# Performance work log

Hardware: AMD Instinct MI355X
Metric: run time of the kernel (lower is better)

## Reference

```python
import jax, jax.numpy as jnp
import numpy as np
from jax import lax

N, L, D = 16, 512, 256
FILT, K = 256, 3
MAXDUR = 8
MEL_MAX = L * (MAXDUR - 1)  # 3584, worst-case sum of durations
LN_EPS = 1e-5


def _conv1d(x, w, b):
    # x: [N, L, Cin], w: [K, Cin, Cout] -> [N, L, Cout], SAME padding (pad=(K-1)//2)
    return lax.conv_general_dilated(x, w, (1,), 'SAME',
                                    dimension_numbers=('NWC', 'WIO', 'NWC')) + b


def _layer_norm(x, g, b):
    mu = jnp.mean(x, axis=-1, keepdims=True)
    var = jnp.var(x, axis=-1, keepdims=True)
    return (x - mu) * lax.rsqrt(var + LN_EPS) * g + b


def _variance_predictor(x, conv1_w, conv1_b, ln1_g, ln1_b,
                        conv2_w, conv2_b, ln2_g, ln2_b, lin_w, lin_b):
    # Standard FastSpeech duration predictor (dropout omitted: eval mode)
    h = _layer_norm(jax.nn.relu(_conv1d(x, conv1_w, conv1_b)), ln1_g, ln1_b)
    h = _layer_norm(jax.nn.relu(_conv1d(h, conv2_w, conv2_b)), ln2_g, ln2_b)
    return (h @ lin_w + lin_b)[..., 0]  # [N, L] log-durations


def setup_inputs() -> dict:
    key = jax.random.key(0)
    ks = jax.random.split(key, 6)
    s = 0.02
    return {
        'x': jax.random.normal(ks[0], (N, L, D), jnp.float32),
        'conv1_w': jax.random.normal(ks[1], (K, D, FILT), jnp.float32) * s,
        'conv1_b': jnp.zeros((FILT,), jnp.float32),
        'ln1_g': jnp.ones((FILT,), jnp.float32),
        'ln1_b': jnp.zeros((FILT,), jnp.float32),
        'conv2_w': jax.random.normal(ks[2], (K, FILT, FILT), jnp.float32) * s,
        'conv2_b': jnp.zeros((FILT,), jnp.float32),
        'ln2_g': jnp.ones((FILT,), jnp.float32),
        'ln2_b': jnp.zeros((FILT,), jnp.float32),
        'lin_w': jax.random.normal(ks[3], (FILT, 1), jnp.float32) * s,
        'lin_b': jnp.zeros((1,), jnp.float32),
        'target': jax.random.randint(ks[4], (N, L), 0, MAXDUR, jnp.int32),
        'mel_max_length': MEL_MAX,
    }


def reference(x, conv1_w, conv1_b, ln1_g, ln1_b, conv2_w, conv2_b,
              ln2_g, ln2_b, lin_w, lin_b, target, mel_max_length):
    log_dur = _variance_predictor(x, conv1_w, conv1_b, ln1_g, ln1_b,
                                  conv2_w, conv2_b, ln2_g, ln2_b, lin_w, lin_b)
    # Dense alignment (faithful to create_alignment), padded directly to mel_max_length
    M = mel_max_length  # static python int
    end = jnp.cumsum(target, axis=1)            # [N, L]
    start = end - target                        # [N, L]
    idx = jnp.arange(M, dtype=target.dtype)[None, :, None]  # [1, M, 1]
    align = ((idx >= start[:, None, :]) & (idx < end[:, None, :])).astype(x.dtype)  # [N, M, L]
    output = jnp.einsum('nml,nld->nmd', align, x)  # [N, M, D]
    return output, log_dur
```

## Files before the change

### kernel.cpp

```cpp
#include <hip/hip_runtime.h>
#include <cstddef>

#define N_ 16
#define L_ 512
#define D_ 256
#define M_ 3584
#define LN_EPS 1e-5f

typedef __attribute__((ext_vector_type(8))) short bf16x8;
typedef __attribute__((ext_vector_type(4))) float f32x4;

__device__ inline unsigned int f2bf_raw(float f) {
    union { float f; unsigned int u; } v; v.f = f;
    return (v.u + 0x7FFFu + ((v.u >> 16) & 1u)) >> 16;
}
__device__ inline unsigned int pack2bf(float lo, float hi) {
    return f2bf_raw(lo) | (f2bf_raw(hi) << 16);
}
__device__ inline float bf2f(unsigned int hw) {
    union { unsigned int u; float f; } v; v.u = hw << 16; return v.f;
}
__device__ inline int aswz(int row, int colb) {
    return row * 512 + (((colb & 0x1F0) ^ ((row & 7) << 4)) | (colb & 0xF));
}

__global__ __launch_bounds__(512)
void prep_kernel(const float* __restrict__ W1, unsigned short* __restrict__ Wt1,
                 const float* __restrict__ W2, unsigned short* __restrict__ Wt2,
                 const int* __restrict__ target, int* __restrict__ idx) {
    __shared__ union { float t[2][32][33]; int s[L_]; } sm;
    const int bid = blockIdx.x;
    if (bid < 192) {
        const int half = threadIdx.x >> 8, st = threadIdx.x & 255;
        const int tile = bid * 2 + half;
        const int kb = (tile % 24) * 32;
        const int cb = ((tile / 24) % 8) * 32;
        const float* W = (tile >= 192) ? W2 : W1;
        unsigned short* Wt = (tile >= 192) ? Wt2 : Wt1;
        const int tx = st & 31, ty = st >> 5;
#pragma unroll
        for (int r = 0; r < 32; r += 8)
            sm.t[half][ty + r][tx] = W[(size_t)(kb + ty + r) * 256 + cb + tx];
        __syncthreads();
        const int jl = st >> 7, l = (st >> 1) & 63, e0 = (st & 1) * 4;
        ushort4 o;
        o.x = (unsigned short)f2bf_raw(sm.t[half][(l >> 4) * 8 + e0 + 0][jl * 16 + (l & 15)]);
        o.y = (unsigned short)f2bf_raw(sm.t[half][(l >> 4) * 8 + e0 + 1][jl * 16 + (l & 15)]);
        o.z = (unsigned short)f2bf_raw(sm.t[half][(l >> 4) * 8 + e0 + 2][jl * 16 + (l & 15)]);
        o.w = (unsigned short)f2bf_raw(sm.t[half][(l >> 4) * 8 + e0 + 3][jl * 16 + (l & 15)]);
        *(ushort4*)(Wt + ((((size_t)(kb >> 5) * 16) + (cb >> 4) + jl) * 64 + l) * 8 + e0) = o;
    } else {
        const int n = bid - 192, t = threadIdx.x;
        const int tv = target[n * L_ + t];
        sm.s[t] = tv;
        __syncthreads();
        for (int off = 1; off < L_; off <<= 1) {
            int v = (t >= off) ? sm.s[t - off] : 0;
            __syncthreads();
            sm.s[t] += v;
            __syncthreads();
        }
        const int e = sm.s[t], st0 = e - tv;
        const int total = sm.s[L_ - 1];
        int* row = idx + (size_t)n * M_;
        for (int j = st0; j < e; ++j) row[j] = t;
        for (int m = total + t; m < M_; m += 512) row[m] = -1;
    }
}

template <int NR, int MAXS>
__device__ __forceinline__ void conv_phase(const unsigned char* Ab,
        const unsigned short* __restrict__ Wf,
        int wv, int lane, int fr, int fg, f32x4 (&acc)[NR][2]) {
    const unsigned short* wb = Wf + ((size_t)(2 * wv) * 64 + lane) * 8;
    uint4 p00 = *(const uint4*)(wb);
    uint4 p01 = *(const uint4*)(wb + 512);
    uint4 p10 = *(const uint4*)(wb + 8192);
    uint4 p11 = *(const uint4*)(wb + 8192 + 512);
    for (int ks = 0; ks < 24; ++ks) {
        uint4 q0, q1;
        if (ks < 22) {
            const unsigned short* wp = wb + (size_t)(ks + 2) * 8192;
            q0 = *(const uint4*)(wp);
            q1 = *(const uint4*)(wp + 512);
        }
        const int cib = (ks & 7) * 64 + fg * 16;
        const int koff = ks >> 3;
        bf16x8 av[NR];
#pragma unroll
        for (int r = 0; r < NR; ++r) {
            int ar = r * 16 + fr + koff;
            if (ar > MAXS) ar = MAXS;
            av[r] = *(const bf16x8*)(Ab + ar * 512 + (cib ^ ((ar & 7) << 4)));
        }
        bf16x8 bb0 = *(bf16x8*)&p00, bb1 = *(bf16x8*)&p01;
        __builtin_amdgcn_s_setprio(1);
#pragma unroll
        for (int r = 0; r < NR; ++r) {
            acc[r][0] = __builtin_amdgcn_mfma_f32_16x16x32_bf16(bb0, av[r], acc[r][0], 0, 0, 0);
            acc[r][1] = __builtin_amdgcn_mfma_f32_16x16x32_bf16(bb1, av[r], acc[r][1], 0, 0, 0);
        }
        __builtin_amdgcn_s_setprio(0);
        p00 = p10; p01 = p11;
        p10 = q0;  p11 = q1;
    }
}

template <int NR, int NROWS>
__device__ __forceinline__ void store_h(unsigned char* Ab, f32x4 (&acc)[NR][2],
        const float* __restrict__ bias, int wv, int fr, int fg) {
#pragma unroll
    for (int r = 0; r < NR; ++r) {
        const int slot = r * 16 + fr;
        if (slot < NROWS) {
#pragma unroll
            for (int j = 0; j < 2; ++j) {
                const int co = wv * 32 + j * 16 + fg * 4;
                const float4 bb = *(const float4*)&bias[co];
                uint2 o;
                o.x = pack2bf(fmaxf(acc[r][j][0] + bb.x, 0.f),
                              fmaxf(acc[r][j][1] + bb.y, 0.f));
                o.y = pack2bf(fmaxf(acc[r][j][2] + bb.z, 0.f),
                              fmaxf(acc[r][j][3] + bb.w, 0.f));
                *(uint2*)(Ab + aswz(slot, 2 * co)) = o;
            }
        }
    }
}

__global__ __launch_bounds__(512, 6)
void mega_kernel(const float* __restrict__ x,
                 const unsigned short* __restrict__ Wf1,
                 const unsigned short* __restrict__ Wf2,
                 const float* __restrict__ b1, const float* __restrict__ g1,
                 const float* __restrict__ be1,
                 const float* __restrict__ b2, const float* __restrict__ g2,
                 const float* __restrict__ be2,
                 const float* __restrict__ lw, const float* __restrict__ lb,
                 const int* __restrict__ idx,
                 float* __restrict__ out0, float* __restrict__ log_dur) {
    __shared__ unsigned char smA[36 * 512];
    const int tid = threadIdx.x, lane = tid & 63, wv = tid >> 6;

    if (blockIdx.x >= 256) {
        const int gb = blockIdx.x - 256;
        const int n = gb >> 5;
        const int m0 = (gb & 31) * 112 + wv;
        const int* ip = idx + (size_t)n * M_ + m0;
        const float* xn = x + (size_t)n * L_ * D_ + lane * 4;
        float* op = out0 + ((size_t)n * M_ + m0) * D_ + lane * 4;
#pragma unroll
        for (int i = 0; i < 7; ++i) {
            const int la = ip[(2 * i) * 8];
            const int lb2 = ip[(2 * i + 1) * 8];
            f32x4 oa = {0.f, 0.f, 0.f, 0.f};
            f32x4 ob = {0.f, 0.f, 0.f, 0.f};
            if (la >= 0)  oa = *(const f32x4*)(xn + (size_t)la * D_);
            if (lb2 >= 0) ob = *(const f32x4*)(xn + (size_t)lb2 * D_);
            __builtin_nontemporal_store(oa, (f32x4*)(op + (size_t)(2 * i) * 8 * D_));
            __builtin_nontemporal_store(ob, (f32x4*)(op + (size_t)(2 * i + 1) * 8 * D_));
        }
        return;
    }

    const int row0 = blockIdx.x * 32;
    const int n = row0 >> 9, l0 = row0 & 511;
    const int fr = lane & 15, fg = lane >> 4;

    for (int i = tid; i < 36 * 64; i += 512) {
        int r = i >> 6, c4 = i & 63;
        int l = l0 - 2 + r;
        float4 v = {0.f, 0.f, 0.f, 0.f};
        if (l >= 0 && l < L_)
            v = ((const float4*)(x + ((size_t)(n * L_ + l)) * D_))[c4];
        uint2 p;
        p.x = pack2bf(v.x, v.y);
        p.y = pack2bf(v.z, v.w);
        *(uint2*)(smA + aswz(r, c4 * 8)) = p;
    }
    __syncthreads();

    f32x4 a1[3][2];
#pragma unroll
    for (int r = 0; r < 3; ++r) { a1[r][0] = (f32x4){0,0,0,0}; a1[r][1] = (f32x4){0,0,0,0}; }
    conv_phase<3, 35>(smA, Wf1, wv, lane, fr, fg, a1);
    __syncthreads();
    store_h<3, 34>(smA, a1, b1, wv, fr, fg);
    __syncthreads();

    {
        const float4 gv = *(const float4*)&g1[lane * 4];
        const float4 bv = *(const float4*)&be1[lane * 4];
        for (int mm = wv; mm < 34; mm += 8) {
            const int addr = aswz(mm, lane * 8);
            const int hrow = l0 - 1 + mm;
            if (hrow < 0 || hrow >= L_) {
                *(uint2*)(smA + addr) = (uint2){0u, 0u};
                continue;
            }
            uint2 pv = *(uint2*)(smA + addr);
            float v0 = bf2f(pv.x & 0xFFFFu), v1 = bf2f(pv.x >> 16);
            float v2 = bf2f(pv.y & 0xFFFFu), v3 = bf2f(pv.y >> 16);
            float s = v0 + v1 + v2 + v3;
            float ss = v0 * v0 + v1 * v1 + v2 * v2 + v3 * v3;
#pragma unroll
            for (int off = 32; off; off >>= 1) {
                s += __shfl_xor(s, off);
                ss += __shfl_xor(ss, off);
            }
            const float mu = s * (1.f / D_);
            const float var = ss * (1.f / D_) - mu * mu;
            const float rs = rsqrtf(var + LN_EPS);
            uint2 o;
            o.x = pack2bf((v0 - mu) * rs * gv.x + bv.x, (v1 - mu) * rs * gv.y + bv.y);
            o.y = pack2bf((v2 - mu) * rs * gv.z + bv.z, (v3 - mu) * rs * gv.w + bv.w);
            *(uint2*)(smA + addr) = o;
        }
    }
    __syncthreads();

    f32x4 a2[2][2];
#pragma unroll
    for (int r = 0; r < 2; ++r) { a2[r][0] = (f32x4){0,0,0,0}; a2[r][1] = (f32x4){0,0,0,0}; }
    conv_phase<2, 33>(smA, Wf2, wv, lane, fr, fg, a2);
    __syncthreads();
    store_h<2, 32>(smA, a2, b2, wv, fr, fg);
    __syncthreads();

    {
        const float4 gv = *(const float4*)&g2[lane * 4];
        const float4 bv = *(const float4*)&be2[lane * 4];
        const float4 wvv = *(const float4*)&lw[lane * 4];
        for (int mm = wv; mm < 32; mm += 8) {
            uint2 pv = *(uint2*)(smA + aswz(mm, lane * 8));
            float v0 = bf2f(pv.x & 0xFFFFu), v1 = bf2f(pv.x >> 16);
            float v2 = bf2f(pv.y & 0xFFFFu), v3 = bf2f(pv.y >> 16);
            float s = v0 + v1 + v2 + v3;
            float ss = v0 * v0 + v1 * v1 + v2 * v2 + v3 * v3;
#pragma unroll
            for (int off = 32; off; off >>= 1) {
                s += __shfl_xor(s, off);
                ss += __shfl_xor(ss, off);
            }
            const float mu = s * (1.f / D_);
            const float var = ss * (1.f / D_) - mu * mu;
            const float rs = rsqrtf(var + LN_EPS);
            float dot = ((v0 - mu) * rs * gv.x + bv.x) * wvv.x
                      + ((v1 - mu) * rs * gv.y + bv.y) * wvv.y
                      + ((v2 - mu) * rs * gv.z + bv.z) * wvv.z
                      + ((v3 - mu) * rs * gv.w + bv.w) * wvv.w;
#pragma unroll
            for (int off = 32; off; off >>= 1) dot += __shfl_xor(dot, off);
            if (lane == 0) log_dur[row0 + mm] = dot + lb[0];
        }
    }
}

extern "C" void kernel_launch(void* const* d_in, const int* in_sizes, int n_in,
                              void* d_out, int out_size, void* d_ws, size_t ws_size,
                              hipStream_t stream) {
    const float* x   = (const float*)d_in[0];
    const float* w1  = (const float*)d_in[1];
    const float* b1  = (const float*)d_in[2];
    const float* g1  = (const float*)d_in[3];
    const float* be1 = (const float*)d_in[4];
    const float* w2  = (const float*)d_in[5];
    const float* b2  = (const float*)d_in[6];
    const float* g2  = (const float*)d_in[7];
    const float* be2 = (const float*)d_in[8];
    const float* lw  = (const float*)d_in[9];
    const float* lb  = (const float*)d_in[10];
    const int* target = (const int*)d_in[11];

    float* out0 = (float*)d_out;
    float* log_dur = out0 + (size_t)N_ * M_ * D_;

    unsigned short* w1f = (unsigned short*)d_ws;
    unsigned short* w2f = w1f + 24 * 8192;
    int* idx = (int*)(w2f + 24 * 8192);

    prep_kernel<<<208, 512, 0, stream>>>(w1, w1f, w2, w2f, target, idx);
    mega_kernel<<<768, 512, 0, stream>>>(x, w1f, w2f, b1, g1, be1,
                                         b2, g2, be2, lw, lb, idx,
                                         out0, log_dur);
}
```

Baseline: 37.21 us.

## Warp-specialize mega kernel: overlap gather writes with conv phases in same block

Result: faster. 33.39 us (-10.3%).

```diff
diff --git a/kernel.cpp b/kernel.cpp
--- a/kernel.cpp
+++ b/kernel.cpp
@@ -128,7 +128,7 @@
     }
 }
 
-__global__ __launch_bounds__(512, 6)
+__global__ __launch_bounds__(1024, 4)
 void mega_kernel(const float* __restrict__ x,
                  const unsigned short* __restrict__ Wf1,
                  const unsigned short* __restrict__ Wf2,
@@ -141,54 +141,57 @@
                  float* __restrict__ out0, float* __restrict__ log_dur) {
     __shared__ unsigned char smA[36 * 512];
     const int tid = threadIdx.x, lane = tid & 63, wv = tid >> 6;
-
-    if (blockIdx.x >= 256) {
-        const int gb = blockIdx.x - 256;
-        const int n = gb >> 5;
-        const int m0 = (gb & 31) * 112 + wv;
-        const int* ip = idx + (size_t)n * M_ + m0;
-        const float* xn = x + (size_t)n * L_ * D_ + lane * 4;
-        float* op = out0 + ((size_t)n * M_ + m0) * D_ + lane * 4;
-#pragma unroll
-        for (int i = 0; i < 7; ++i) {
-            const int la = ip[(2 * i) * 8];
-            const int lb2 = ip[(2 * i + 1) * 8];
-            f32x4 oa = {0.f, 0.f, 0.f, 0.f};
-            f32x4 ob = {0.f, 0.f, 0.f, 0.f};
-            if (la >= 0)  oa = *(const f32x4*)(xn + (size_t)la * D_);
-            if (lb2 >= 0) ob = *(const f32x4*)(xn + (size_t)lb2 * D_);
-            __builtin_nontemporal_store(oa, (f32x4*)(op + (size_t)(2 * i) * 8 * D_));
-            __builtin_nontemporal_store(ob, (f32x4*)(op + (size_t)(2 * i + 1) * 8 * D_));
-        }
-        return;
-    }
-
-    const int row0 = blockIdx.x * 32;
+    const int bid = blockIdx.x;
+    const bool is_conv = (wv < 8);
+
+    const int row0 = bid * 32;
     const int n = row0 >> 9, l0 = row0 & 511;
     const int fr = lane & 15, fg = lane >> 4;
 
-    for (int i = tid; i < 36 * 64; i += 512) {
-        int r = i >> 6, c4 = i & 63;
-        int l = l0 - 2 + r;
-        float4 v = {0.f, 0.f, 0.f, 0.f};
-        if (l >= 0 && l < L_)
-            v = ((const float4*)(x + ((size_t)(n * L_ + l)) * D_))[c4];
-        uint2 p;
-        p.x = pack2bf(v.x, v.y);
-        p.y = pack2bf(v.z, v.w);
-        *(uint2*)(smA + aswz(r, c4 * 8)) = p;
-    }
-    __syncthreads();
+    const int gwv = wv - 8;
+    const int m0 = (bid & 15) * 224 + gwv;
+    const int* ip = idx + (size_t)n * M_ + m0;
+    const float* xn = x + (size_t)n * L_ * D_ + lane * 4;
+    float* op = out0 + ((size_t)n * M_ + m0) * D_ + lane * 4;
+    auto gchunk = [&](int i0, int i1) {
+        for (int i = i0; i < i1; ++i) {
+            const int li = ip[i * 8];
+            f32x4 o = {0.f, 0.f, 0.f, 0.f};
+            if (li >= 0) o = *(const f32x4*)(xn + (size_t)li * D_);
+            *(f32x4*)(op + (size_t)i * 8 * D_) = o;
+        }
+    };
 
     f32x4 a1[3][2];
 #pragma unroll
     for (int r = 0; r < 3; ++r) { a1[r][0] = (f32x4){0,0,0,0}; a1[r][1] = (f32x4){0,0,0,0}; }
-    conv_phase<3, 35>(smA, Wf1, wv, lane, fr, fg, a1);
-    __syncthreads();
-    store_h<3, 34>(smA, a1, b1, wv, fr, fg);
-    __syncthreads();
-
-    {
+
+    if (is_conv) {
+        for (int i = tid; i < 36 * 64; i += 512) {
+            int r = i >> 6, c4 = i & 63;
+            int l = l0 - 2 + r;
+            float4 v = {0.f, 0.f, 0.f, 0.f};
+            if (l >= 0 && l < L_)
+                v = ((const float4*)(x + ((size_t)(n * L_ + l)) * D_))[c4];
+            uint2 p;
+            p.x = pack2bf(v.x, v.y);
+            p.y = pack2bf(v.z, v.w);
+            *(uint2*)(smA + aswz(r, c4 * 8)) = p;
+        }
+    } else {
+        gchunk(0, 5);
+    }
+    __syncthreads();
+
+    if (is_conv) conv_phase<3, 35>(smA, Wf1, wv, lane, fr, fg, a1);
+    else gchunk(5, 10);
+    __syncthreads();
+
+    if (is_conv) store_h<3, 34>(smA, a1, b1, wv, fr, fg);
+    else gchunk(10, 15);
+    __syncthreads();
+
+    if (is_conv) {
         const float4 gv = *(const float4*)&g1[lane * 4];
         const float4 bv = *(const float4*)&be1[lane * 4];
         for (int mm = wv; mm < 34; mm += 8) {
@@ -216,18 +219,23 @@
             o.y = pack2bf((v2 - mu) * rs * gv.z + bv.z, (v3 - mu) * rs * gv.w + bv.w);
             *(uint2*)(smA + addr) = o;
         }
+    } else {
+        gchunk(15, 20);
     }
     __syncthreads();
 
     f32x4 a2[2][2];
 #pragma unroll
     for (int r = 0; r < 2; ++r) { a2[r][0] = (f32x4){0,0,0,0}; a2[r][1] = (f32x4){0,0,0,0}; }
-    conv_phase<2, 33>(smA, Wf2, wv, lane, fr, fg, a2);
-    __syncthreads();
-    store_h<2, 32>(smA, a2, b2, wv, fr, fg);
-    __syncthreads();
-
-    {
+    if (is_conv) conv_phase<2, 33>(smA, Wf2, wv, lane, fr, fg, a2);
+    else gchunk(20, 24);
+    __syncthreads();
+
+    if (is_conv) store_h<2, 32>(smA, a2, b2, wv, fr, fg);
+    else gchunk(24, 28);
+    __syncthreads();
+
+    if (is_conv) {
         const float4 gv = *(const float4*)&g2[lane * 4];
         const float4 bv = *(const float4*)&be2[lane * 4];
         const float4 wvv = *(const float4*)&lw[lane * 4];
@@ -280,7 +288,7 @@
     int* idx = (int*)(w2f + 24 * 8192);
 
     prep_kernel<<<208, 512, 0, stream>>>(w1, w1f, w2, w2f, target, idx);
-    mega_kernel<<<768, 512, 0, stream>>>(x, w1f, w2f, b1, g1, be1,
-                                         b2, g2, be2, lw, lb, idx,
-                                         out0, log_dur);
-}
+    mega_kernel<<<256, 1024, 0, stream>>>(x, w1f, w2f, b1, g1, be1,
+                                          b2, g2, be2, lw, lb, idx,
+                                          out0, log_dur);
+}
```

## Merge gather and conv blocks into 256 blocks of 1024 threads

Applied to the files above, without the earlier changes.

Measured after the change: 35.95 us. -3.4%, faster.

```diff
diff --git a/kernel.cpp b/kernel.cpp
--- a/kernel.cpp
+++ b/kernel.cpp
@@ -71,19 +71,13 @@
 template <int NR, int MAXS>
 __device__ __forceinline__ void conv_phase(const unsigned char* Ab,
         const unsigned short* __restrict__ Wf,
-        int wv, int lane, int fr, int fg, f32x4 (&acc)[NR][2]) {
-    const unsigned short* wb = Wf + ((size_t)(2 * wv) * 64 + lane) * 8;
-    uint4 p00 = *(const uint4*)(wb);
-    uint4 p01 = *(const uint4*)(wb + 512);
-    uint4 p10 = *(const uint4*)(wb + 8192);
-    uint4 p11 = *(const uint4*)(wb + 8192 + 512);
+        int wv, int lane, int fr, int fg, f32x4 (&acc)[NR]) {
+    const unsigned short* wb = Wf + ((size_t)wv * 64 + lane) * 8;
+    uint4 p0 = *(const uint4*)(wb);
+    uint4 p1 = *(const uint4*)(wb + 8192);
     for (int ks = 0; ks < 24; ++ks) {
-        uint4 q0, q1;
-        if (ks < 22) {
-            const unsigned short* wp = wb + (size_t)(ks + 2) * 8192;
-            q0 = *(const uint4*)(wp);
-            q1 = *(const uint4*)(wp + 512);
-        }
+        uint4 q;
+        if (ks < 22) q = *(const uint4*)(wb + (size_t)(ks + 2) * 8192);
         const int cib = (ks & 7) * 64 + fg * 16;
         const int koff = ks >> 3;
         bf16x8 av[NR];
@@ -93,42 +87,34 @@
             if (ar > MAXS) ar = MAXS;
             av[r] = *(const bf16x8*)(Ab + ar * 512 + (cib ^ ((ar & 7) << 4)));
         }
-        bf16x8 bb0 = *(bf16x8*)&p00, bb1 = *(bf16x8*)&p01;
+        bf16x8 bb = *(bf16x8*)&p0;
         __builtin_amdgcn_s_setprio(1);
 #pragma unroll
-        for (int r = 0; r < NR; ++r) {
-            acc[r][0] = __builtin_amdgcn_mfma_f32_16x16x32_bf16(bb0, av[r], acc[r][0], 0, 0, 0);
-            acc[r][1] = __builtin_amdgcn_mfma_f32_16x16x32_bf16(bb1, av[r], acc[r][1], 0, 0, 0);
-        }
+        for (int r = 0; r < NR; ++r)
+            acc[r] = __builtin_amdgcn_mfma_f32_16x16x32_bf16(bb, av[r], acc[r], 0, 0, 0);
         __builtin_amdgcn_s_setprio(0);
-        p00 = p10; p01 = p11;
-        p10 = q0;  p11 = q1;
+        p0 = p1; p1 = q;
     }
 }
 
 template <int NR, int NROWS>
-__device__ __forceinline__ void store_h(unsigned char* Ab, f32x4 (&acc)[NR][2],
+__device__ __forceinline__ void store_h(unsigned char* Ab, f32x4 (&acc)[NR],
         const float* __restrict__ bias, int wv, int fr, int fg) {
+    const int co = wv * 16 + fg * 4;
+    const float4 bb = *(const float4*)&bias[co];
 #pragma unroll
     for (int r = 0; r < NR; ++r) {
         const int slot = r * 16 + fr;
         if (slot < NROWS) {
-#pragma unroll
-            for (int j = 0; j < 2; ++j) {
-                const int co = wv * 32 + j * 16 + fg * 4;
-                const float4 bb = *(const float4*)&bias[co];
-                uint2 o;
-                o.x = pack2bf(fmaxf(acc[r][j][0] + bb.x, 0.f),
-                              fmaxf(acc[r][j][1] + bb.y, 0.f));
-                o.y = pack2bf(fmaxf(acc[r][j][2] + bb.z, 0.f),
-                              fmaxf(acc[r][j][3] + bb.w, 0.f));
-                *(uint2*)(Ab + aswz(slot, 2 * co)) = o;
-            }
-        }
-    }
-}
-
-__global__ __launch_bounds__(512, 6)
+            uint2 o;
+            o.x = pack2bf(fmaxf(acc[r][0] + bb.x, 0.f), fmaxf(acc[r][1] + bb.y, 0.f));
+            o.y = pack2bf(fmaxf(acc[r][2] + bb.z, 0.f), fmaxf(acc[r][3] + bb.w, 0.f));
+            *(uint2*)(Ab + aswz(slot, 2 * co)) = o;
+        }
+    }
+}
+
+__global__ __launch_bounds__(1024, 4)
 void mega_kernel(const float* __restrict__ x,
                  const unsigned short* __restrict__ Wf1,
                  const unsigned short* __restrict__ Wf2,
@@ -141,33 +127,26 @@
                  float* __restrict__ out0, float* __restrict__ log_dur) {
     __shared__ unsigned char smA[36 * 512];
     const int tid = threadIdx.x, lane = tid & 63, wv = tid >> 6;
-
-    if (blockIdx.x >= 256) {
-        const int gb = blockIdx.x - 256;
-        const int n = gb >> 5;
-        const int m0 = (gb & 31) * 112 + wv;
+    const int bid = blockIdx.x;
+    const int row0 = bid * 32;
+    const int n = row0 >> 9, l0 = row0 & 511;
+    const int fr = lane & 15, fg = lane >> 4;
+
+    {
+        const int m0 = (bid & 15) * 224 + wv;
         const int* ip = idx + (size_t)n * M_ + m0;
         const float* xn = x + (size_t)n * L_ * D_ + lane * 4;
         float* op = out0 + ((size_t)n * M_ + m0) * D_ + lane * 4;
 #pragma unroll
-        for (int i = 0; i < 7; ++i) {
-            const int la = ip[(2 * i) * 8];
-            const int lb2 = ip[(2 * i + 1) * 8];
-            f32x4 oa = {0.f, 0.f, 0.f, 0.f};
-            f32x4 ob = {0.f, 0.f, 0.f, 0.f};
-            if (la >= 0)  oa = *(const f32x4*)(xn + (size_t)la * D_);
-            if (lb2 >= 0) ob = *(const f32x4*)(xn + (size_t)lb2 * D_);
-            __builtin_nontemporal_store(oa, (f32x4*)(op + (size_t)(2 * i) * 8 * D_));
-            __builtin_nontemporal_store(ob, (f32x4*)(op + (size_t)(2 * i + 1) * 8 * D_));
-        }
-        return;
-    }
-
-    const int row0 = blockIdx.x * 32;
-    const int n = row0 >> 9, l0 = row0 & 511;
-    const int fr = lane & 15, fg = lane >> 4;
-
-    for (int i = tid; i < 36 * 64; i += 512) {
+        for (int i = 0; i < 14; ++i) {
+            const int li = ip[i * 16];
+            f32x4 o = {0.f, 0.f, 0.f, 0.f};
+            if (li >= 0) o = *(const f32x4*)(xn + (size_t)li * D_);
+            __builtin_nontemporal_store(o, (f32x4*)(op + (size_t)i * 16 * D_));
+        }
+    }
+
+    for (int i = tid; i < 36 * 64; i += 1024) {
         int r = i >> 6, c4 = i & 63;
         int l = l0 - 2 + r;
         float4 v = {0.f, 0.f, 0.f, 0.f};
@@ -180,9 +159,9 @@
     }
     __syncthreads();
 
-    f32x4 a1[3][2];
-#pragma unroll
-    for (int r = 0; r < 3; ++r) { a1[r][0] = (f32x4){0,0,0,0}; a1[r][1] = (f32x4){0,0,0,0}; }
+    f32x4 a1[3];
+#pragma unroll
+    for (int r = 0; r < 3; ++r) a1[r] = (f32x4){0.f, 0.f, 0.f, 0.f};
     conv_phase<3, 35>(smA, Wf1, wv, lane, fr, fg, a1);
     __syncthreads();
     store_h<3, 34>(smA, a1, b1, wv, fr, fg);
@@ -191,7 +170,7 @@
     {
         const float4 gv = *(const float4*)&g1[lane * 4];
         const float4 bv = *(const float4*)&be1[lane * 4];
-        for (int mm = wv; mm < 34; mm += 8) {
+        for (int mm = wv; mm < 34; mm += 16) {
             const int addr = aswz(mm, lane * 8);
             const int hrow = l0 - 1 + mm;
             if (hrow < 0 || hrow >= L_) {
@@ -219,9 +198,9 @@
     }
     __syncthreads();
 
-    f32x4 a2[2][2];
-#pragma unroll
-    for (int r = 0; r < 2; ++r) { a2[r][0] = (f32x4){0,0,0,0}; a2[r][1] = (f32x4){0,0,0,0}; }
+    f32x4 a2[2];
+#pragma unroll
+    for (int r = 0; r < 2; ++r) a2[r] = (f32x4){0.f, 0.f, 0.f, 0.f};
     conv_phase<2, 33>(smA, Wf2, wv, lane, fr, fg, a2);
     __syncthreads();
     store_h<2, 32>(smA, a2, b2, wv, fr, fg);
@@ -231,7 +210,7 @@
         const float4 gv = *(const float4*)&g2[lane * 4];
         const float4 bv = *(const float4*)&be2[lane * 4];
         const float4 wvv = *(const float4*)&lw[lane * 4];
-        for (int mm = wv; mm < 32; mm += 8) {
+        for (int mm = wv; mm < 32; mm += 16) {
             uint2 pv = *(uint2*)(smA + aswz(mm, lane * 8));
             float v0 = bf2f(pv.x & 0xFFFFu), v1 = bf2f(pv.x >> 16);
             float v2 = bf2f(pv.y & 0xFFFFu), v3 = bf2f(pv.y >> 16);
@@ -280,7 +259,7 @@
     int* idx = (int*)(w2f + 24 * 8192);
 
     prep_kernel<<<208, 512, 0, stream>>>(w1, w1f, w2, w2f, target, idx);
-    mega_kernel<<<768, 512, 0, stream>>>(x, w1f, w2f, b1, g1, be1,
-                                         b2, g2, be2, lw, lb, idx,
-                                         out0, log_dur);
-}
+    mega_kernel<<<256, 1024, 0, stream>>>(x, w1f, w2f, b1, g1, be1,
+                                          b2, g2, be2, lw, lb, idx,
+                                          out0, log_dur);
+}
```
